# Kernel tuning notes

Hardware: AMD Instinct MI355X
Metric: run time of the kernel (lower is better)

Reference implementation:

```python
import jax, jax.numpy as jnp
import numpy as np

B, L, INPUT_DIM = 32, 1024, 4
M1 = M2 = 256
D_STATE, D_CONV, EXPAND = 16, 4, 2
D_INNER = EXPAND * M1          # 512
DT_RANK = M1 // 16             # ceil(256/16) = 16
EPS = 1e-5


def silu(x):
    return x * jax.nn.sigmoid(x)


def layernorm(x, g, b):
    mu = jnp.mean(x, axis=-1, keepdims=True)
    var = jnp.mean(jnp.square(x - mu), axis=-1, keepdims=True)
    return (x - mu) * jax.lax.rsqrt(var + EPS) * g + b


def mamba_block(x, in_w, conv_w, conv_b, xproj_w, dt_w, dt_b, A_log, D, out_w):
    # x: (B, L, d_model)
    Bb, Ll, _ = x.shape
    d_inner, d_conv = conv_w.shape
    d_state = A_log.shape[1]
    dt_rank = dt_w.shape[1]

    xz = x @ in_w.T                      # (B, L, 2*d_inner)
    xi, z = jnp.split(xz, 2, axis=-1)

    # depthwise causal conv1d, kernel size d_conv
    xpad = jnp.pad(xi, ((0, 0), (d_conv - 1, 0), (0, 0)))
    xc = conv_b + sum(conv_w[:, k] * xpad[:, k:k + Ll, :] for k in range(d_conv))
    xc = silu(xc)                        # (B, L, d_inner)

    dbc = xc @ xproj_w.T                 # (B, L, dt_rank + 2*d_state)
    dt, Bm, Cm = jnp.split(dbc, [dt_rank, dt_rank + d_state], axis=-1)
    dt = jax.nn.softplus(dt @ dt_w.T + dt_b)  # (B, L, d_inner)
    A = -jnp.exp(A_log)                  # (d_inner, d_state)

    def step(h, inp):
        dt_t, B_t, C_t, x_t = inp        # (B,di) (B,ds) (B,ds) (B,di)
        dA = jnp.exp(dt_t[:, :, None] * A)                       # (B,di,ds)
        h = dA * h + (dt_t * x_t)[:, :, None] * B_t[:, None, :]  # (B,di,ds)
        y = jnp.einsum('bds,bs->bd', h, C_t)                     # (B,di)
        return h, y

    h0 = jnp.zeros((Bb, d_inner, d_state), dtype=x.dtype)
    xs = (jnp.swapaxes(dt, 0, 1), jnp.swapaxes(Bm, 0, 1),
          jnp.swapaxes(Cm, 0, 1), jnp.swapaxes(xc, 0, 1))
    _, ys = jax.lax.scan(step, h0, xs)
    y = jnp.swapaxes(ys, 0, 1) + xc * D  # (B, L, d_inner)
    y = y * silu(z)
    return y @ out_w.T                   # (B, L, d_model)


def setup_inputs() -> dict:
    key = jax.random.key(0)
    ks = iter(jax.random.split(key, 40))
    n = lambda shape, s=0.02: (jax.random.normal(next(ks), shape, jnp.float32) * s)

    def mamba_params(d_model):
        di = EXPAND * d_model
        return dict(
            in_w=n((2 * di, d_model)),
            conv_w=n((di, D_CONV), 0.2),
            conv_b=n((di,)),
            xproj_w=n((DT_RANK + 2 * D_STATE, di)),
            dt_w=n((di, DT_RANK), 0.1),
            dt_b=n((di,), 0.1),
            A_log=jnp.log(jnp.tile(jnp.arange(1, D_STATE + 1, dtype=jnp.float32), (di, 1))),
            D=jnp.ones((di,), jnp.float32),
            out_w=n((d_model, di)),
        )

    m1 = mamba_params(M1)
    m2 = mamba_params(M2)
    inp = {
        'x_seq': jax.random.normal(next(ks), (B, L, INPUT_DIM), jnp.float32),
        'x_static': jax.random.normal(next(ks), (B, 5), jnp.float32),
        'p1_w': n((M1, INPUT_DIM), 0.2), 'p1_b': n((M1,)),
        'ln1_g': jnp.ones((M1,), jnp.float32), 'ln1_b': jnp.zeros((M1,), jnp.float32),
        'p2_w': n((M2, M1)), 'p2_b': n((M2,)),
        'ln2_g': jnp.ones((M2,), jnp.float32), 'ln2_b': jnp.zeros((M2,), jnp.float32),
        'h1_w': n((M2 // 2, M2 + 5), 0.1), 'h1_b': n((M2 // 2,)),
        'h2_w': n((1, M2 // 2), 0.1), 'h2_b': n((1,)),
    }
    for name, p in (('m1', m1), ('m2', m2)):
        for k, v in p.items():
            inp[f'{name}_{k}'] = v
    return inp


def reference(x_seq, x_static,
              p1_w, p1_b, ln1_g, ln1_b,
              p2_w, p2_b, ln2_g, ln2_b,
              h1_w, h1_b, h2_w, h2_b,
              m1_in_w, m1_conv_w, m1_conv_b, m1_xproj_w, m1_dt_w, m1_dt_b, m1_A_log, m1_D, m1_out_w,
              m2_in_w, m2_conv_w, m2_conv_b, m2_xproj_w, m2_dt_w, m2_dt_b, m2_A_log, m2_D, m2_out_w):
    x = x_seq @ p1_w.T + p1_b
    x = layernorm(x, ln1_g, ln1_b)
    x = mamba_block(x, m1_in_w, m1_conv_w, m1_conv_b, m1_xproj_w, m1_dt_w, m1_dt_b, m1_A_log, m1_D, m1_out_w)
    x = x @ p2_w.T + p2_b
    x = layernorm(x, ln2_g, ln2_b)
    x = mamba_block(x, m2_in_w, m2_conv_w, m2_conv_b, m2_xproj_w, m2_dt_w, m2_dt_b, m2_A_log, m2_D, m2_out_w)
    x = jnp.mean(x, axis=1)                    # (B, M2)
    x = jnp.concatenate([x, x_static], axis=-1)
    x = jax.nn.elu(x @ h1_w.T + h1_b)
    out = x @ h2_w.T + h2_b                    # (B, 1)
    return out[..., 0]
```

## Files before the change

### kernel.cpp

```cpp
#include <hip/hip_runtime.h>
#include <math.h>

#define NB 32
#define L  1024
#define CH 512
#define NCH (L / CH)
#define RC (NB * CH)
#define DM 256
#define DI 512
#define DS 16
#define SCT 16
#define NSC (CH / SCT)
#define LOG2E 1.44269504f
#define LN2   0.69314718f

typedef short short8 __attribute__((ext_vector_type(8)));
typedef float f32x4 __attribute__((ext_vector_type(4)));
typedef unsigned short u16;

__device__ inline unsigned f2bf_u(float x) {
    unsigned u = __float_as_uint(x);
    return (u + 0x7fffu + ((u >> 16) & 1u)) >> 16;
}


__global__ __launch_bounds__(256) void k_p1_ln(
    const float* __restrict__ xseq, const float* __restrict__ w,
    const float* __restrict__ bias, const float* __restrict__ g,
    const float* __restrict__ bb, u16* __restrict__ outh, u16* __restrict__ outl,
    int t0)
{
    int r  = blockIdx.x;
    int b  = r & 31;
    int tl = r >> 5;
    int m  = threadIdx.x;
    const float* xr = xseq + ((size_t)b * L + t0 + tl) * 4;
    float x0 = xr[0], x1 = xr[1], x2 = xr[2], x3 = xr[3];
    const float* wr = w + m * 4;
    float v = bias[m] + x0 * wr[0] + x1 * wr[1] + x2 * wr[2] + x3 * wr[3];

    __shared__ float s1[4], s2[4];
    float a = v, bq = v * v;
    for (int o = 32; o > 0; o >>= 1) { a += __shfl_down(a, o); bq += __shfl_down(bq, o); }
    int wid = m >> 6, lane = m & 63;
    if (lane == 0) { s1[wid] = a; s2[wid] = bq; }
    __syncthreads();
    if (m == 0) {
        s1[0] = s1[0] + s1[1] + s1[2] + s1[3];
        s2[0] = s2[0] + s2[1] + s2[2] + s2[3];
    }
    __syncthreads();
    float mu  = s1[0] * (1.f / 256.f);
    float var = s2[0] * (1.f / 256.f) - mu * mu;
    float o2 = (v - mu) * rsqrtf(var + 1e-5f) * g[m] + bb[m];
    unsigned hb = f2bf_u(o2);
    outh[(size_t)r * 256 + m] = (u16)hb;
    outl[(size_t)r * 256 + m] = (u16)f2bf_u(o2 - __uint_as_float(hb << 16));
}

__global__ __launch_bounds__(256) void k_ln(
    const float* __restrict__ in, const float* __restrict__ g,
    const float* __restrict__ bb, u16* __restrict__ outh, u16* __restrict__ outl)
{
    int r = blockIdx.x;
    int m = threadIdx.x;
    float v = in[(size_t)r * 256 + m];

    __shared__ float s1[4], s2[4];
    float a = v, bq = v * v;
    for (int o = 32; o > 0; o >>= 1) { a += __shfl_down(a, o); bq += __shfl_down(bq, o); }
    int wid = m >> 6, lane = m & 63;
    if (lane == 0) { s1[wid] = a; s2[wid] = bq; }
    __syncthreads();
    if (m == 0) {
        s1[0] = s1[0] + s1[1] + s1[2] + s1[3];
        s2[0] = s2[0] + s2[1] + s2[2] + s2[3];
    }
    __syncthreads();
    float mu  = s1[0] * (1.f / 256.f);
    float var = s2[0] * (1.f / 256.f) - mu * mu;
    float o2 = (v - mu) * rsqrtf(var + 1e-5f) * g[m] + bb[m];
    unsigned hb = f2bf_u(o2);
    outh[(size_t)r * 256 + m] = (u16)hb;
    outl[(size_t)r * 256 + m] = (u16)f2bf_u(o2 - __uint_as_float(hb << 16));
}

__global__ __launch_bounds__(256) void k_wcvt_all(
    const float* __restrict__ w1i, const float* __restrict__ w1o,
    const float* __restrict__ w2i, const float* __restrict__ w2o,
    const float* __restrict__ p2,
    u16* __restrict__ o1ih, u16* __restrict__ o1il,
    u16* __restrict__ o1oh, u16* __restrict__ o1ol,
    u16* __restrict__ o2ih, u16* __restrict__ o2il,
    u16* __restrict__ o2oh, u16* __restrict__ o2ol,
    u16* __restrict__ op2h, u16* __restrict__ op2l)
{
    int i = blockIdx.x * 256 + threadIdx.x;
    const float* src; u16 *oh, *ol; int j;
    if (i < 262144)      { src = w1i; oh = o1ih; ol = o1il; j = i; }
    else if (i < 393216) { src = w1o; oh = o1oh; ol = o1ol; j = i - 262144; }
    else if (i < 655360) { src = w2i; oh = o2ih; ol = o2il; j = i - 393216; }
    else if (i < 786432) { src = w2o; oh = o2oh; ol = o2ol; j = i - 655360; }
    else                 { src = p2;  oh = op2h; ol = op2l; j = i - 786432; }
    float v = src[j];
    unsigned hb = f2bf_u(v);
    oh[j] = (u16)hb;
    ol[j] = (u16)f2bf_u(v - __uint_as_float(hb << 16));
}

template <int OUTK, bool BIAS>
__global__ __launch_bounds__(256) void k_gmfma(
    const u16* __restrict__ Ahg, const u16* __restrict__ Alg, int lda,
    const u16* __restrict__ Whg, const u16* __restrict__ Wlg,
    const float* __restrict__ bias, void* __restrict__ C0, void* __restrict__ C1,
    int N, int K)
{
    __shared__ u16 Ah[128 * 40], Al[128 * 40];
    __shared__ u16 Wh[128 * 40], Wl[128 * 40];

    int tid = threadIdx.x;
    int wv = tid >> 6, ln = tid & 63;
    int wr = wv >> 1, wc = wv & 1;
    int m0 = blockIdx.x * 128, n0 = blockIdx.y * 128;
    int sr = tid >> 1, sk = (tid & 1) << 4;
    int frow = ln & 15, fk = (ln >> 4) << 3;

    f32x4 acc[4][4] = {};

    for (int k0 = 0; k0 < K; k0 += 32) {
        const u16* ah = Ahg + (size_t)(m0 + sr) * lda + k0 + sk;
        const u16* al = Alg + (size_t)(m0 + sr) * lda + k0 + sk;
        const u16* wh = Whg + (size_t)(n0 + sr) * K + k0 + sk;
        const u16* wl = Wlg + (size_t)(n0 + sr) * K + k0 + sk;
        short8 vah0 = *(const short8*)ah, vah1 = *(const short8*)(ah + 8);
        short8 val0 = *(const short8*)al, val1 = *(const short8*)(al + 8);
        short8 vwh0 = *(const short8*)wh, vwh1 = *(const short8*)(wh + 8);
        short8 vwl0 = *(const short8*)wl, vwl1 = *(const short8*)(wl + 8);

        __syncthreads();

        *(short8*)&Ah[sr * 40 + sk]     = vah0;
        *(short8*)&Ah[sr * 40 + sk + 8] = vah1;
        *(short8*)&Al[sr * 40 + sk]     = val0;
        *(short8*)&Al[sr * 40 + sk + 8] = val1;
        *(short8*)&Wh[sr * 40 + sk]     = vwh0;
        *(short8*)&Wh[sr * 40 + sk + 8] = vwh1;
        *(short8*)&Wl[sr * 40 + sk]     = vwl0;
        *(short8*)&Wl[sr * 40 + sk + 8] = vwl1;

        __syncthreads();

        short8 afh[4], afl[4], wfh[4], wfl[4];
#pragma unroll
        for (int g = 0; g < 4; g++) {
            int ra = (wr * 64 + g * 16 + frow) * 40 + fk;
            int rw = (wc * 64 + g * 16 + frow) * 40 + fk;
            afh[g] = *(const short8*)&Ah[ra];
            afl[g] = *(const short8*)&Al[ra];
            wfh[g] = *(const short8*)&Wh[rw];
            wfl[g] = *(const short8*)&Wl[rw];
        }
#pragma unroll
        for (int mg = 0; mg < 4; mg++)
#pragma unroll
            for (int ng = 0; ng < 4; ng++) {
                acc[mg][ng] = __builtin_amdgcn_mfma_f32_16x16x32_bf16(afh[mg], wfh[ng], acc[mg][ng], 0, 0, 0);
                acc[mg][ng] = __builtin_amdgcn_mfma_f32_16x16x32_bf16(afh[mg], wfl[ng], acc[mg][ng], 0, 0, 0);
                acc[mg][ng] = __builtin_amdgcn_mfma_f32_16x16x32_bf16(afl[mg], wfh[ng], acc[mg][ng], 0, 0, 0);
            }
    }

#pragma unroll
    for (int ng = 0; ng < 4; ng++) {
        int col = n0 + wc * 64 + ng * 16 + frow;
        float bv = BIAS ? bias[col] : 0.f;
#pragma unroll
        for (int mg = 0; mg < 4; mg++)
#pragma unroll
            for (int r = 0; r < 4; r++) {
                int row = m0 + wr * 64 + mg * 16 + (ln >> 4) * 4 + r;
                float v = acc[mg][ng][r] + bv;
                if (OUTK == 0) {
                    ((float*)C0)[(size_t)row * N + col] = v;
                } else {
                    unsigned hb = f2bf_u(v);
                    ((u16*)C0)[(size_t)row * N + col] = (u16)hb;
                    ((u16*)C1)[(size_t)row * N + col] =
                        (u16)f2bf_u(v - __uint_as_float(hb << 16));
                }
            }
    }
}

__global__ __launch_bounds__(256) void k_xpart(
    const float* __restrict__ A, const float* __restrict__ W,
    float* __restrict__ Cpart, int M, int K, int kcnt)
{
    const int BM = 64, BK = 16;
    __shared__ float As[BK][BM];
    __shared__ float Ws[BK][64];

    int m0   = blockIdx.x * BM;
    int kbeg = blockIdx.y * kcnt;
    int tid = threadIdx.x;
    int tx  = tid & 15, ty = tid >> 4;
    int lr  = tid >> 2;
    int lc  = (tid & 3) * 4;

    float acc[4][4] = {};

    for (int k0 = kbeg; k0 < kbeg + kcnt; k0 += BK) {
        float4 av = *(const float4*)(A + (size_t)(m0 + lr) * K + k0 + lc);
        As[lc + 0][lr] = av.x; As[lc + 1][lr] = av.y;
        As[lc + 2][lr] = av.z; As[lc + 3][lr] = av.w;
        float4 wv = make_float4(0.f, 0.f, 0.f, 0.f);
        if (lr < 48) wv = *(const float4*)(W + (size_t)lr * K + k0 + lc);
        Ws[lc + 0][lr] = wv.x; Ws[lc + 1][lr] = wv.y;
        Ws[lc + 2][lr] = wv.z; Ws[lc + 3][lr] = wv.w;
        __syncthreads();
#pragma unroll
        for (int k = 0; k < BK; k++) {
            float a[4], bv[4];
            *(float4*)a  = *(const float4*)&As[k][ty * 4];
            *(float4*)bv = *(const float4*)&Ws[k][tx * 4];
#pragma unroll
            for (int i = 0; i < 4; i++)
#pragma unroll
                for (int j = 0; j < 4; j++)
                    acc[i][j] = fmaf(a[i], bv[j], acc[i][j]);
        }
        __syncthreads();
    }

    int n = tx * 4;
    if (n < 48) {
        float* cp = Cpart + (size_t)blockIdx.y * M * 48;
#pragma unroll
        for (int i = 0; i < 4; i++) {
            float4 v = make_float4(acc[i][0], acc[i][1], acc[i][2], acc[i][3]);
            *(float4*)(cp + (size_t)(m0 + ty * 4 + i) * 48 + n) = v;
        }
    }
}

__global__ __launch_bounds__(256) void k_conv(
    const float* __restrict__ xz, float* __restrict__ halo,
    const float* __restrict__ cw, const float* __restrict__ cb,
    float* __restrict__ xc, int t0, int save_halo)
{
    size_t i4 = ((size_t)blockIdx.x * 256 + threadIdx.x) * 4;
    int d  = (int)(i4 & 511);
    int r  = (int)(i4 >> 9);
    int b  = r & 31;
    int tl = r >> 5;

    float4 w0 = *(const float4*)(cw + (d + 0) * 4);
    float4 w1 = *(const float4*)(cw + (d + 1) * 4);
    float4 w2 = *(const float4*)(cw + (d + 2) * 4);
    float4 w3 = *(const float4*)(cw + (d + 3) * 4);
    float4 acc = *(const float4*)(cb + d);
    float4 vlast = make_float4(0.f, 0.f, 0.f, 0.f);

#pragma unroll
    for (int k = 0; k < 4; k++) {
        int tsl = tl - 3 + k;
        float4 v;
        if (tsl >= 0)
            v = *(const float4*)(xz + ((size_t)tsl * 32 + b) * 1024 + d);
        else if (t0 + tsl >= 0)
            v = *(const float4*)(halo + ((size_t)(tsl + 3) * 32 + b) * 512 + d);
        else
            continue;
        if (k == 3) vlast = v;
        acc.x = fmaf((&w0.x)[k], v.x, acc.x);
        acc.y = fmaf((&w1.x)[k], v.y, acc.y);
        acc.z = fmaf((&w2.x)[k], v.z, acc.z);
        acc.w = fmaf((&w3.x)[k], v.w, acc.w);
    }
    float4 o;
    o.x = acc.x / (1.f + __expf(-acc.x));
    o.y = acc.y / (1.f + __expf(-acc.y));
    o.z = acc.z / (1.f + __expf(-acc.z));
    o.w = acc.w / (1.f + __expf(-acc.w));
    *(float4*)(xc + i4) = o;

    if (save_halo && tl >= CH - 3)
        *(float4*)(halo + ((size_t)(tl - (CH - 3)) * 32 + b) * 512 + d) = vlast;
}

__global__ __launch_bounds__(256) void k_scanA(
    const float* __restrict__ xc, const float* __restrict__ part,
    const float* __restrict__ dtw, const float* __restrict__ dtb,
    const float* __restrict__ A_log,
    float* __restrict__ hend, float* __restrict__ sumdt)
{
    int bx = blockIdx.x;
    int b    = bx >> 6;
    int half = (bx >> 5) & 1;
    int c    = bx & 31;
    int d = (half << 8) + threadIdx.x;

    float A2[DS], h[DS], wdt[DS];
#pragma unroll
    for (int s = 0; s < DS; s++) {
        A2[s] = -__expf(A_log[d * DS + s]) * LOG2E;
        h[s] = 0.f;
        wdt[s] = dtw[d * DS + s];
    }
    float dtbv = dtb[d];
    float A20 = A2[0];
    float A0nat = A20 * LN2;
    bool geo = true;
#pragma unroll
    for (int s = 0; s < DS; s++)
        geo = geo && (fabsf(A2[s] - (float)(s + 1) * A20) <=
                      1e-5f * fabsf(A2[s]) + 1e-30f);

    __shared__ float Bs[SCT][48];
    {
        const size_t st = (size_t)RC * 48;
        for (int f = threadIdx.x; f < SCT * 48; f += 256) {
            int tt = f / 48, jj = f - tt * 48;
            size_t base = ((size_t)(c * SCT + tt) * 32 + b) * 48 + jj;
            Bs[tt][jj] = (part[base] + part[st + base]) +
                         (part[2 * st + base] + part[3 * st + base]);
        }
    }
    __syncthreads();

    float cum = 0.f;
    if (geo) {
        for (int tt = 0; tt < SCT; tt++) {
            size_t idx = ((size_t)(c * SCT + tt) * 32 + b) * DI + d;
            float p0 = 0.f, p1 = 0.f, p2 = 0.f, p3 = 0.f;
#pragma unroll
            for (int k = 0; k < 4; k++) {
                p0 = fmaf(Bs[tt][k],      wdt[k],      p0);
                p1 = fmaf(Bs[tt][4 + k],  wdt[4 + k],  p1);
                p2 = fmaf(Bs[tt][8 + k],  wdt[8 + k],  p2);
                p3 = fmaf(Bs[tt][12 + k], wdt[12 + k], p3);
            }
            float s0 = dtbv + ((p0 + p1) + (p2 + p3));
            float u  = __expf(s0);
            float t2 = __log2f(1.f + u);
            if (s0 > 80.f) t2 = s0 * LOG2E;
            float dt = LN2 * t2;
            cum += dt;
            float dtx = dt * xc[idx];
            float q  = exp2f(t2 * A0nat);
            float q2 = q * q, q3 = q2 * q, q4 = q2 * q2;
            float pv[4] = { q, q2, q3, q4 };
            float r = 1.f;
#pragma unroll
            for (int g = 0; g < 4; g++) {
#pragma unroll
                for (int j = 0; j < 4; j++) {
                    int s = g * 4 + j;
                    float dA = r * pv[j];
                    h[s] = fmaf(dA, h[s], dtx * Bs[tt][16 + s]);
                }
                r *= q4;
            }
        }
    } else {
        for (int tt = 0; tt < SCT; tt++) {
            size_t idx = ((size_t)(c * SCT + tt) * 32 + b) * DI + d;
            float s0 = dtbv;
#pragma unroll
            for (int k = 0; k < DS; k++) s0 = fmaf(Bs[tt][k], wdt[k], s0);
            float dt = (s0 > 20.f) ? s0 : log1pf(expf(s0));
            cum += dt;
            float dtx = dt * xc[idx];
#pragma unroll
            for (int s = 0; s < DS; s++) {
                float dA = exp2f(dt * A2[s]);
                h[s] = fmaf(dA, h[s], dtx * Bs[tt][16 + s]);
            }
        }
    }
    float* hp = hend + ((size_t)(c * 32 + b) * 512 + d) * DS;
#pragma unroll
    for (int s = 0; s < DS; s++) hp[s] = h[s];
    sumdt[((size_t)c * 32 + b) * 512 + d] = cum;
}

__global__ __launch_bounds__(256) void k_scanB(
    const float* __restrict__ sumdt, float* __restrict__ hend,
    const float* __restrict__ A_log, float* __restrict__ hs, int first)
{
    int id = blockIdx.x * 256 + threadIdx.x;
    int s = id & 15;
    int d = (id >> 4) & 511;
    int b = id >> 13;
    float A2 = -__expf(A_log[d * DS + s]) * LOG2E;
    size_t hsi = ((size_t)(b << 9) + d) * DS + s;
    float hin = first ? 0.f : hs[hsi];
    for (int c = 0; c < NSC; c++) {
        size_t hi = ((size_t)(c * 32 + b) * 512 + d) * DS + s;
        float he = hend[hi];
        float sd = sumdt[((size_t)c * 32 + b) * 512 + d];
        hend[hi] = hin;
        hin = fmaf(exp2f(A2 * sd), hin, he);
    }
    hs[hsi] = hin;
}

__global__ __launch_bounds__(256) void k_scanC(
    const float* __restrict__ xc, const float* __restrict__ part,
    const float* __restrict__ dtw, const float* __restrict__ dtb,
    const float* __restrict__ xz,
    const float* __restrict__ A_log, const float* __restrict__ Dp,
    const float* __restrict__ hinit,
    u16* __restrict__ yh, u16* __restrict__ yl)
{
    int bx = blockIdx.x;
    int b    = bx >> 6;
    int half = (bx >> 5) & 1;
    int c    = bx & 31;
    int d = (half << 8) + threadIdx.x;

    float A2[DS], h[DS], wdt[DS];
    const float* hp = hinit + ((size_t)(c * 32 + b) * 512 + d) * DS;
#pragma unroll
    for (int s = 0; s < DS; s++) {
        A2[s] = -__expf(A_log[d * DS + s]) * LOG2E;
        h[s] = hp[s];
        wdt[s] = dtw[d * DS + s];
    }
    float dtbv = dtb[d];
    float Dv = Dp[d];
    float A20 = A2[0];
    float A0nat = A20 * LN2;
    bool geo = true;
#pragma unroll
    for (int s = 0; s < DS; s++)
        geo = geo && (fabsf(A2[s] - (float)(s + 1) * A20) <=
                      1e-5f * fabsf(A2[s]) + 1e-30f);

    __shared__ float BC[SCT][48];
    {
        const size_t st = (size_t)RC * 48;
        for (int f = threadIdx.x; f < SCT * 48; f += 256) {
            int tt = f / 48, jj = f - tt * 48;
            size_t base = ((size_t)(c * SCT + tt) * 32 + b) * 48 + jj;
            BC[tt][jj] = (part[base] + part[st + base]) +
                         (part[2 * st + base] + part[3 * st + base]);
        }
    }
    __syncthreads();

    if (geo) {
        for (int tt = 0; tt < SCT; tt++) {
            size_t row = (size_t)(c * SCT + tt) * 32 + b;
            size_t idx = row * DI + d;
            float p0 = 0.f, p1 = 0.f, p2 = 0.f, p3 = 0.f;
#pragma unroll
            for (int k = 0; k < 4; k++) {
                p0 = fmaf(BC[tt][k],      wdt[k],      p0);
                p1 = fmaf(BC[tt][4 + k],  wdt[4 + k],  p1);
                p2 = fmaf(BC[tt][8 + k],  wdt[8 + k],  p2);
                p3 = fmaf(BC[tt][12 + k], wdt[12 + k], p3);
            }
            float s0 = dtbv + ((p0 + p1) + (p2 + p3));
            float u  = __expf(s0);
            float t2 = __log2f(1.f + u);
            if (s0 > 80.f) t2 = s0 * LOG2E;
            float dt = LN2 * t2;
            float x  = xc[idx];
            float z  = xz[(row << 10) + 512 + d];
            float dtx = dt * x;
            float y = 0.f;
            float q  = exp2f(t2 * A0nat);
            float q2 = q * q, q3 = q2 * q, q4 = q2 * q2;
            float pv[4] = { q, q2, q3, q4 };
            float r = 1.f;
#pragma unroll
            for (int g = 0; g < 4; g++) {
#pragma unroll
                for (int j = 0; j < 4; j++) {
                    int s = g * 4 + j;
                    float dA = r * pv[j];
                    h[s] = fmaf(dA, h[s], dtx * BC[tt][16 + s]);
                    y = fmaf(h[s], BC[tt][32 + s], y);
                }
                r *= q4;
            }
            float yact = (y + x * Dv) * (z / (1.f + __expf(-z)));
            unsigned hb = f2bf_u(yact);
            yh[row * DI + d] = (u16)hb;
            yl[row * DI + d] = (u16)f2bf_u(yact - __uint_as_float(hb << 16));
        }
    } else {
        for (int tt = 0; tt < SCT; tt++) {
            size_t row = (size_t)(c * SCT + tt) * 32 + b;
            size_t idx = row * DI + d;
            float s0 = dtbv;
#pragma unroll
            for (int k = 0; k < DS; k++) s0 = fmaf(BC[tt][k], wdt[k], s0);
            float dt = (s0 > 20.f) ? s0 : log1pf(expf(s0));
            float x  = xc[idx];
            float z  = xz[(row << 10) + 512 + d];
            float dtx = dt * x;
            float y = 0.f;
#pragma unroll
            for (int s = 0; s < DS; s++) {
                float dA = exp2f(dt * A2[s]);
                h[s] = fmaf(dA, h[s], dtx * BC[tt][16 + s]);
                y = fmaf(h[s], BC[tt][32 + s], y);
            }
            float yact = (y + x * Dv) * (z / (1.f + __expf(-z)));
            unsigned hb = f2bf_u(yact);
            yh[row * DI + d] = (u16)hb;
            yl[row * DI + d] = (u16)f2bf_u(yact - __uint_as_float(hb << 16));
        }
    }
}

__global__ __launch_bounds__(256) void k_meanacc(
    const float* __restrict__ mo, float* __restrict__ macc, int first)
{
    int b = blockIdx.x, g = blockIdx.y;
    int m = threadIdx.x;
    float s = 0.f;
    const int TLP = CH / 8;
    for (int t = 0; t < TLP; t++) {
        int tl = g * TLP + t;
        s += mo[((size_t)tl * 32 + b) * 256 + m];
    }
    int i = (b * 8 + g) * 256 + m;
    if (first) macc[i] = s;
    else       macc[i] += s;
}

__global__ __launch_bounds__(128) void k_head(
    const float* __restrict__ macc, const float* __restrict__ xst,
    const float* __restrict__ h1w, const float* __restrict__ h1b,
    const float* __restrict__ h2w, const float* __restrict__ h2b,
    float* __restrict__ out)
{
    int b = blockIdx.x;
    int j = threadIdx.x;
    const float* wr = h1w + j * 261;
    const float* mr = macc + (size_t)b * 8 * 256;
    float s = h1b[j];
    for (int k = 0; k < 256; k++) {
        float mv = 0.f;
#pragma unroll
        for (int g = 0; g < 8; g++) mv += mr[g * 256 + k];
        s = fmaf(mv * (1.f / 1024.f), wr[k], s);
    }
    for (int k = 0; k < 5; k++) s = fmaf(xst[b * 5 + k], wr[256 + k], s);
    float e = (s > 0.f) ? s : expm1f(s);

    __shared__ float sb[128];
    sb[j] = e * h2w[j];
    __syncthreads();
    for (int o = 64; o > 0; o >>= 1) {
        if (j < o) sb[j] += sb[j + o];
        __syncthreads();
    }
    if (j == 0) out[b] = sb[0] + h2b[0];
}

static void run_mamba_chunk(hipStream_t stream,
                            const u16* x1h, const u16* x1l, void* const* P,
                            const u16* wih, const u16* wil,
                            const u16* woh, const u16* wol, int out_pairs,
                            float* xzc, float* xcc, float* xpartb,
                            float* moc, u16* moh, u16* mol,
                            u16* yh, u16* yl,
                            float* hendb, float* sumdtb, float* halo,
                            float* hstate, int t0, int save_halo)
{
    const float* cw     = (const float*)P[1];
    const float* cb     = (const float*)P[2];
    const float* xpw    = (const float*)P[3];
    const float* dtw    = (const float*)P[4];
    const float* dtbias = (const float*)P[5];
    const float* Alog   = (const float*)P[6];
    const float* Dp     = (const float*)P[7];
    int first = (t0 == 0);

    k_gmfma<0, false><<<dim3(RC / 128, 1024 / 128), 256, 0, stream>>>(
        x1h, x1l, 256, wih, wil, nullptr, xzc, nullptr, 1024, 256);
    k_conv<<<RC * DI / 1024, 256, 0, stream>>>(xzc, halo, cw, cb, xcc, t0, save_halo);
    k_xpart<<<dim3(RC / 64, 4), 256, 0, stream>>>(xcc, xpw, xpartb, RC, 512, 128);
    k_scanA<<<32 * 2 * NSC, 256, 0, stream>>>(xcc, xpartb, dtw, dtbias, Alog,
                                              hendb, sumdtb);
    k_scanB<<<32 * 512 * DS / 256, 256, 0, stream>>>(sumdtb, hendb, Alog, hstate, first);
    k_scanC<<<32 * 2 * NSC, 256, 0, stream>>>(xcc, xpartb, dtw, dtbias, xzc,
                                              Alog, Dp, hendb, yh, yl);
    if (out_pairs)
        k_gmfma<1, false><<<dim3(RC / 128, 256 / 128), 256, 0, stream>>>(
            yh, yl, 512, woh, wol, nullptr, moh, mol, 256, 512);
    else
        k_gmfma<0, false><<<dim3(RC / 128, 256 / 128), 256, 0, stream>>>(
            yh, yl, 512, woh, wol, nullptr, moc, nullptr, 256, 512);
}

extern "C" void kernel_launch(void* const* d_in, const int* in_sizes, int n_in,
                              void* d_out, int out_size, void* d_ws, size_t ws_size,
                              hipStream_t stream)
{
    const float* xseq = (const float*)d_in[0];
    const float* xst  = (const float*)d_in[1];
    const float* p1w  = (const float*)d_in[2];
    const float* p1b  = (const float*)d_in[3];
    const float* ln1g = (const float*)d_in[4];
    const float* ln1b = (const float*)d_in[5];
    const float* p2w  = (const float*)d_in[6];
    const float* p2b  = (const float*)d_in[7];
    const float* ln2g = (const float*)d_in[8];
    const float* ln2b = (const float*)d_in[9];
    const float* h1w  = (const float*)d_in[10];
    const float* h1b  = (const float*)d_in[11];
    const float* h2w  = (const float*)d_in[12];
    const float* h2b  = (const float*)d_in[13];

    float* ws = (float*)d_ws;
    float* xzc    = ws;
    float* xcc    = xzc  + (size_t)RC * 1024;
    float* moc    = xcc  + (size_t)RC * 512;
    u16*   x1h    = (u16*)(moc + (size_t)RC * 256);
    u16*   x1l    = x1h + (size_t)RC * 256;
    float* hendb  = moc;
    float* after  = (float*)(x1l + (size_t)RC * 256);
    u16*   yh     = (u16*)after;
    u16*   yl     = yh + (size_t)RC * 512;
    u16*   moh    = yl + (size_t)RC * 512;
    u16*   mol    = moh + (size_t)RC * 256;
    float* sumdtb = (float*)(mol + (size_t)RC * 256);
    float* halo1  = sumdtb + NSC * 32 * 512;
    float* halo2  = halo1 + 3 * 32 * 512;
    float* hs1    = halo2 + 3 * 32 * 512;
    float* hs2    = hs1  + 32 * 512 * DS;
    float* macc   = hs2  + 32 * 512 * DS;
    u16*   wm1ih  = (u16*)(macc + 32 * 8 * 256);
    u16*   wm1il  = wm1ih + 262144;
    u16*   wm1oh  = wm1il + 262144;
    u16*   wm1ol  = wm1oh + 131072;
    u16*   wm2ih  = wm1ol + 131072;
    u16*   wm2il  = wm2ih + 262144;
    u16*   wm2oh  = wm2il + 262144;
    u16*   wm2ol  = wm2oh + 131072;
    u16*   wp2h   = wm2ol + 131072;
    u16*   wp2l   = wp2h + 65536;
    float* xpartb = (float*)(wp2l + 65536);
    size_t need = (size_t)((char*)(xpartb + 4 * (size_t)RC * 48) - (char*)ws);
    if (ws_size < need) return;

    k_wcvt_all<<<3332, 256, 0, stream>>>(
        (const float*)d_in[14], (const float*)d_in[22],
        (const float*)d_in[23], (const float*)d_in[31], p2w,
        wm1ih, wm1il, wm1oh, wm1ol, wm2ih, wm2il, wm2oh, wm2ol, wp2h, wp2l);

    for (int c = 0; c < NCH; c++) {
        int t0 = c * CH;
        int first = (c == 0);
        int save_halo = (c != NCH - 1);

        k_p1_ln<<<RC, 256, 0, stream>>>(xseq, p1w, p1b, ln1g, ln1b, x1h, x1l, t0);

        run_mamba_chunk(stream, x1h, x1l, d_in + 14, wm1ih, wm1il, wm1oh, wm1ol, 1,
                        xzc, xcc, xpartb, moc, moh, mol, yh, yl,
                        hendb, sumdtb, halo1, hs1, t0, save_halo);

        k_gmfma<0, true><<<dim3(RC / 128, 256 / 128), 256, 0, stream>>>(
            moh, mol, 256, wp2h, wp2l, p2b, xzc, nullptr, 256, 256);
        k_ln<<<RC, 256, 0, stream>>>(xzc, ln2g, ln2b, x1h, x1l);

        run_mamba_chunk(stream, x1h, x1l, d_in + 23, wm2ih, wm2il, wm2oh, wm2ol, 0,
                        xzc, xcc, xpartb, moc, moh, mol, yh, yl,
                        hendb, sumdtb, halo2, hs2, t0, save_halo);

        k_meanacc<<<dim3(NB, 8), 256, 0, stream>>>(moc, macc, first);
    }

    k_head<<<NB, 128, 0, stream>>>(macc, xst, h1w, h1b, h2w, h2b, (float*)d_out);
}
```

Baseline: 839.9 us.

## Fold out-projections into p2 weights and post-mean head projection

Precomputes the product of p2 weight and the first mamba out-projection so the first out GEMM and the p2 GEMM become a single K=512 GEMM on the scan output. For the second mamba block the out-projection is applied after the sequence mean, in a small pre-head kernel, instead of to every token. This removes two full-size GEMMs per chunk and their intermediate buffers, at the cost of a per-call weight-product kernel and a different rounding order.

```diff
diff --git a/kernel.cpp b/kernel.cpp
--- a/kernel.cpp
+++ b/kernel.cpp
@@ -85,34 +85,41 @@
     outl[(size_t)r * 256 + m] = (u16)f2bf_u(o2 - __uint_as_float(hb << 16));
 }
 
-__global__ __launch_bounds__(256) void k_wcvt_all(
-    const float* __restrict__ w1i, const float* __restrict__ w1o,
-    const float* __restrict__ w2i, const float* __restrict__ w2o,
-    const float* __restrict__ p2,
-    u16* __restrict__ o1ih, u16* __restrict__ o1il,
-    u16* __restrict__ o1oh, u16* __restrict__ o1ol,
-    u16* __restrict__ o2ih, u16* __restrict__ o2il,
-    u16* __restrict__ o2oh, u16* __restrict__ o2ol,
-    u16* __restrict__ op2h, u16* __restrict__ op2l)
+__global__ __launch_bounds__(256) void k_wcvt2(
+    const float* __restrict__ w1i, const float* __restrict__ w2i,
+    u16* __restrict__ o1h, u16* __restrict__ o1l,
+    u16* __restrict__ o2h, u16* __restrict__ o2l)
 {
     int i = blockIdx.x * 256 + threadIdx.x;
     const float* src; u16 *oh, *ol; int j;
-    if (i < 262144)      { src = w1i; oh = o1ih; ol = o1il; j = i; }
-    else if (i < 393216) { src = w1o; oh = o1oh; ol = o1ol; j = i - 262144; }
-    else if (i < 655360) { src = w2i; oh = o2ih; ol = o2il; j = i - 393216; }
-    else if (i < 786432) { src = w2o; oh = o2oh; ol = o2ol; j = i - 655360; }
-    else                 { src = p2;  oh = op2h; ol = op2l; j = i - 786432; }
+    if (i < 262144) { src = w1i; oh = o1h; ol = o1l; j = i; }
+    else            { src = w2i; oh = o2h; ol = o2l; j = i - 262144; }
     float v = src[j];
     unsigned hb = f2bf_u(v);
     oh[j] = (u16)hb;
     ol[j] = (u16)f2bf_u(v - __uint_as_float(hb << 16));
 }
 
-template <int OUTK, bool BIAS>
+__global__ __launch_bounds__(256) void k_wcomb(
+    const float* __restrict__ p2w, const float* __restrict__ outw,
+    u16* __restrict__ och, u16* __restrict__ ocl)
+{
+    int idx = blockIdx.x * 256 + threadIdx.x;
+    int n = idx >> 9, k = idx & 511;
+    const float* pr = p2w + n * 256;
+    float s = 0.f;
+    for (int j = 0; j < 256; j++)
+        s = fmaf(pr[j], outw[(size_t)j * 512 + k], s);
+    unsigned hb = f2bf_u(s);
+    och[idx] = (u16)hb;
+    ocl[idx] = (u16)f2bf_u(s - __uint_as_float(hb << 16));
+}
+
+template <bool BIAS>
 __global__ __launch_bounds__(256) void k_gmfma(
     const u16* __restrict__ Ahg, const u16* __restrict__ Alg, int lda,
     const u16* __restrict__ Whg, const u16* __restrict__ Wlg,
-    const float* __restrict__ bias, void* __restrict__ C0, void* __restrict__ C1,
+    const float* __restrict__ bias, float* __restrict__ C0,
     int N, int K)
 {
     __shared__ u16 Ah[128 * 40], Al[128 * 40];
@@ -179,15 +186,7 @@
 #pragma unroll
             for (int r = 0; r < 4; r++) {
                 int row = m0 + wr * 64 + mg * 16 + (ln >> 4) * 4 + r;
-                float v = acc[mg][ng][r] + bv;
-                if (OUTK == 0) {
-                    ((float*)C0)[(size_t)row * N + col] = v;
-                } else {
-                    unsigned hb = f2bf_u(v);
-                    ((u16*)C0)[(size_t)row * N + col] = (u16)hb;
-                    ((u16*)C1)[(size_t)row * N + col] =
-                        (u16)f2bf_u(v - __uint_as_float(hb << 16));
-                }
+                C0[(size_t)row * N + col] = acc[mg][ng][r] + bv;
             }
     }
 }
@@ -516,24 +515,52 @@
     }
 }
 
-__global__ __launch_bounds__(256) void k_meanacc(
-    const float* __restrict__ mo, float* __restrict__ macc, int first)
+__global__ __launch_bounds__(512) void k_meanacc(
+    const u16* __restrict__ yh, const u16* __restrict__ yl,
+    float* __restrict__ macc, int first)
 {
     int b = blockIdx.x, g = blockIdx.y;
-    int m = threadIdx.x;
+    int q = threadIdx.x;
     float s = 0.f;
     const int TLP = CH / 8;
     for (int t = 0; t < TLP; t++) {
-        int tl = g * TLP + t;
-        s += mo[((size_t)tl * 32 + b) * 256 + m];
-    }
-    int i = (b * 8 + g) * 256 + m;
+        size_t i = ((size_t)(g * TLP + t) * 32 + b) * 512 + q;
+        s += __uint_as_float((unsigned)yh[i] << 16) +
+             __uint_as_float((unsigned)yl[i] << 16);
+    }
+    int i = (b * 8 + g) * 512 + q;
     if (first) macc[i] = s;
     else       macc[i] += s;
 }
 
+__global__ __launch_bounds__(256) void k_prehead(
+    const float* __restrict__ macc, const float* __restrict__ wo2,
+    float* __restrict__ mm)
+{
+    int b = blockIdx.x;
+    int n = threadIdx.x;
+    __shared__ float ys[512];
+    for (int q = threadIdx.x; q < 512; q += 256) {
+        float s = 0.f;
+#pragma unroll
+        for (int g = 0; g < 8; g++) s += macc[(b * 8 + g) * 512 + q];
+        ys[q] = s;
+    }
+    __syncthreads();
+    const float* wr = wo2 + (size_t)n * 512;
+    float s = 0.f;
+    for (int q = 0; q < 512; q += 4) {
+        float4 w = *(const float4*)(wr + q);
+        s = fmaf(w.x, ys[q + 0], s);
+        s = fmaf(w.y, ys[q + 1], s);
+        s = fmaf(w.z, ys[q + 2], s);
+        s = fmaf(w.w, ys[q + 3], s);
+    }
+    mm[b * 256 + n] = s * (1.f / 1024.f);
+}
+
 __global__ __launch_bounds__(128) void k_head(
-    const float* __restrict__ macc, const float* __restrict__ xst,
+    const float* __restrict__ mm, const float* __restrict__ xst,
     const float* __restrict__ h1w, const float* __restrict__ h1b,
     const float* __restrict__ h2w, const float* __restrict__ h2b,
     float* __restrict__ out)
@@ -541,14 +568,9 @@
     int b = blockIdx.x;
     int j = threadIdx.x;
     const float* wr = h1w + j * 261;
-    const float* mr = macc + (size_t)b * 8 * 256;
+    const float* mr = mm + b * 256;
     float s = h1b[j];
-    for (int k = 0; k < 256; k++) {
-        float mv = 0.f;
-#pragma unroll
-        for (int g = 0; g < 8; g++) mv += mr[g * 256 + k];
-        s = fmaf(mv * (1.f / 1024.f), wr[k], s);
-    }
+    for (int k = 0; k < 256; k++) s = fmaf(mr[k], wr[k], s);
     for (int k = 0; k < 5; k++) s = fmaf(xst[b * 5 + k], wr[256 + k], s);
     float e = (s > 0.f) ? s : expm1f(s);
 
@@ -562,15 +584,13 @@
     if (j == 0) out[b] = sb[0] + h2b[0];
 }
 
-static void run_mamba_chunk(hipStream_t stream,
-                            const u16* x1h, const u16* x1l, void* const* P,
-                            const u16* wih, const u16* wil,
-                            const u16* woh, const u16* wol, int out_pairs,
-                            float* xzc, float* xcc, float* xpartb,
-                            float* moc, u16* moh, u16* mol,
-                            u16* yh, u16* yl,
-                            float* hendb, float* sumdtb, float* halo,
-                            float* hstate, int t0, int save_halo)
+static void run_mamba_core(hipStream_t stream,
+                           const u16* x1h, const u16* x1l, void* const* P,
+                           const u16* wih, const u16* wil,
+                           float* xzc, float* xcc, float* xpartb,
+                           u16* yh, u16* yl,
+                           float* hendb, float* sumdtb, float* halo,
+                           float* hstate, int t0, int save_halo)
 {
     const float* cw     = (const float*)P[1];
     const float* cb     = (const float*)P[2];
@@ -581,8 +601,8 @@
     const float* Dp     = (const float*)P[7];
     int first = (t0 == 0);
 
-    k_gmfma<0, false><<<dim3(RC / 128, 1024 / 128), 256, 0, stream>>>(
-        x1h, x1l, 256, wih, wil, nullptr, xzc, nullptr, 1024, 256);
+    k_gmfma<false><<<dim3(RC / 128, 1024 / 128), 256, 0, stream>>>(
+        x1h, x1l, 256, wih, wil, nullptr, xzc, 1024, 256);
     k_conv<<<RC * DI / 1024, 256, 0, stream>>>(xzc, halo, cw, cb, xcc, t0, save_halo);
     k_xpart<<<dim3(RC / 64, 4), 256, 0, stream>>>(xcc, xpw, xpartb, RC, 512, 128);
     k_scanA<<<32 * 2 * NSC, 256, 0, stream>>>(xcc, xpartb, dtw, dtbias, Alog,
@@ -590,12 +610,6 @@
     k_scanB<<<32 * 512 * DS / 256, 256, 0, stream>>>(sumdtb, hendb, Alog, hstate, first);
     k_scanC<<<32 * 2 * NSC, 256, 0, stream>>>(xcc, xpartb, dtw, dtbias, xzc,
                                               Alog, Dp, hendb, yh, yl);
-    if (out_pairs)
-        k_gmfma<1, false><<<dim3(RC / 128, 256 / 128), 256, 0, stream>>>(
-            yh, yl, 512, woh, wol, nullptr, moh, mol, 256, 512);
-    else
-        k_gmfma<0, false><<<dim3(RC / 128, 256 / 128), 256, 0, stream>>>(
-            yh, yl, 512, woh, wol, nullptr, moc, nullptr, 256, 512);
 }
 
 extern "C" void kernel_launch(void* const* d_in, const int* in_sizes, int n_in,
@@ -616,43 +630,38 @@
     const float* h1b  = (const float*)d_in[11];
     const float* h2w  = (const float*)d_in[12];
     const float* h2b  = (const float*)d_in[13];
+    const float* wo1  = (const float*)d_in[22];
+    const float* wo2  = (const float*)d_in[31];
 
     float* ws = (float*)d_ws;
     float* xzc    = ws;
     float* xcc    = xzc  + (size_t)RC * 1024;
-    float* moc    = xcc  + (size_t)RC * 512;
-    u16*   x1h    = (u16*)(moc + (size_t)RC * 256);
+    float* hendb  = xcc  + (size_t)RC * 512;
+    u16*   x1h    = (u16*)hendb;
     u16*   x1l    = x1h + (size_t)RC * 256;
-    float* hendb  = moc;
-    float* after  = (float*)(x1l + (size_t)RC * 256);
-    u16*   yh     = (u16*)after;
+    u16*   yh     = (u16*)(hendb + (size_t)RC * 512);
     u16*   yl     = yh + (size_t)RC * 512;
-    u16*   moh    = yl + (size_t)RC * 512;
-    u16*   mol    = moh + (size_t)RC * 256;
-    float* sumdtb = (float*)(mol + (size_t)RC * 256);
+    float* sumdtb = (float*)(yl + (size_t)RC * 512);
     float* halo1  = sumdtb + NSC * 32 * 512;
     float* halo2  = halo1 + 3 * 32 * 512;
     float* hs1    = halo2 + 3 * 32 * 512;
     float* hs2    = hs1  + 32 * 512 * DS;
     float* macc   = hs2  + 32 * 512 * DS;
-    u16*   wm1ih  = (u16*)(macc + 32 * 8 * 256);
+    float* mm     = macc + 32 * 8 * 512;
+    u16*   wm1ih  = (u16*)(mm + 32 * 256);
     u16*   wm1il  = wm1ih + 262144;
-    u16*   wm1oh  = wm1il + 262144;
-    u16*   wm1ol  = wm1oh + 131072;
-    u16*   wm2ih  = wm1ol + 131072;
+    u16*   wm2ih  = wm1il + 262144;
     u16*   wm2il  = wm2ih + 262144;
-    u16*   wm2oh  = wm2il + 262144;
-    u16*   wm2ol  = wm2oh + 131072;
-    u16*   wp2h   = wm2ol + 131072;
-    u16*   wp2l   = wp2h + 65536;
-    float* xpartb = (float*)(wp2l + 65536);
+    u16*   wch    = wm2il + 262144;
+    u16*   wcl    = wch + 131072;
+    float* xpartb = (float*)(wcl + 131072);
     size_t need = (size_t)((char*)(xpartb + 4 * (size_t)RC * 48) - (char*)ws);
     if (ws_size < need) return;
 
-    k_wcvt_all<<<3332, 256, 0, stream>>>(
-        (const float*)d_in[14], (const float*)d_in[22],
-        (const float*)d_in[23], (const float*)d_in[31], p2w,
-        wm1ih, wm1il, wm1oh, wm1ol, wm2ih, wm2il, wm2oh, wm2ol, wp2h, wp2l);
+    k_wcvt2<<<2048, 256, 0, stream>>>(
+        (const float*)d_in[14], (const float*)d_in[23],
+        wm1ih, wm1il, wm2ih, wm2il);
+    k_wcomb<<<512, 256, 0, stream>>>(p2w, wo1, wch, wcl);
 
     for (int c = 0; c < NCH; c++) {
         int t0 = c * CH;
@@ -661,20 +670,21 @@
 
         k_p1_ln<<<RC, 256, 0, stream>>>(xseq, p1w, p1b, ln1g, ln1b, x1h, x1l, t0);
 
-        run_mamba_chunk(stream, x1h, x1l, d_in + 14, wm1ih, wm1il, wm1oh, wm1ol, 1,
-                        xzc, xcc, xpartb, moc, moh, mol, yh, yl,
-                        hendb, sumdtb, halo1, hs1, t0, save_halo);
-
-        k_gmfma<0, true><<<dim3(RC / 128, 256 / 128), 256, 0, stream>>>(
-            moh, mol, 256, wp2h, wp2l, p2b, xzc, nullptr, 256, 256);
+        run_mamba_core(stream, x1h, x1l, d_in + 14, wm1ih, wm1il,
+                       xzc, xcc, xpartb, yh, yl,
+                       hendb, sumdtb, halo1, hs1, t0, save_halo);
+
+        k_gmfma<true><<<dim3(RC / 128, 256 / 128), 256, 0, stream>>>(
+            yh, yl, 512, wch, wcl, p2b, xzc, 256, 512);
         k_ln<<<RC, 256, 0, stream>>>(xzc, ln2g, ln2b, x1h, x1l);
 
-        run_mamba_chunk(stream, x1h, x1l, d_in + 23, wm2ih, wm2il, wm2oh, wm2ol, 0,
-                        xzc, xcc, xpartb, moc, moh, mol, yh, yl,
-                        hendb, sumdtb, halo2, hs2, t0, save_halo);
-
-        k_meanacc<<<dim3(NB, 8), 256, 0, stream>>>(moc, macc, first);
-    }
-
-    k_head<<<NB, 128, 0, stream>>>(macc, xst, h1w, h1b, h2w, h2b, (float*)d_out);
-}
+        run_mamba_core(stream, x1h, x1l, d_in + 23, wm2ih, wm2il,
+                       xzc, xcc, xpartb, yh, yl,
+                       hendb, sumdtb, halo2, hs2, t0, save_halo);
+
+        k_meanacc<<<dim3(NB, 8), 512, 0, stream>>>(yh, yl, macc, first);
+    }
+
+    k_prehead<<<NB, 256, 0, stream>>>(macc, wo2, mm);
+    k_head<<<NB, 128, 0, stream>>>(mm, xst, h1w, h1b, h2w, h2b, (float*)d_out);
+}
```

After: 780.3 us. 7.1% less time.
